# Kernel optimization log

Hardware: AMD Instinct MI355X
Metric: run time of the kernel (lower is better)

## Reference

```python
import jax, jax.numpy as jnp
import numpy as np
from jax import lax

NUM_CLASSES = 80
STRIDES = (8, 16, 32)
CENTER_RADIUS = 2.5
CANDIDATE_K = 10


def setup_inputs() -> dict:
    key = jax.random.key(0)
    ks = jax.random.split(key, 6)
    B, G, NGT = 32, 50, 20
    out0 = jax.random.normal(ks[0], (B, 85, 80, 80), jnp.float32)
    out1 = jax.random.normal(ks[1], (B, 85, 40, 40), jnp.float32)
    out2 = jax.random.normal(ks[2], (B, 85, 20, 20), jnp.float32)
    cls = jax.random.randint(ks[3], (B, G, 1), 0, NUM_CLASSES).astype(jnp.float32)
    cxcy = jax.random.uniform(ks[4], (B, G, 2), minval=32.0, maxval=608.0)
    wh = jax.random.uniform(ks[5], (B, G, 2), minval=16.0, maxval=128.0)
    labels = jnp.concatenate([cls, cxcy, wh], -1)
    valid = (jnp.arange(G) < NGT)[None, :, None]
    labels = labels * valid  # padded rows are all-zero, as the torch code expects
    return {"out0": out0, "out1": out1, "out2": out2, "labels": labels}


def _decode(out, stride):
    # out: [B, 85, H, W] -> [B, H*W, 85] with xy=(pred+grid)*stride, wh=exp(pred)*stride
    B, C, H, W = out.shape
    o = out.transpose(0, 2, 3, 1).reshape(B, H * W, C)
    yv, xv = jnp.meshgrid(jnp.arange(H), jnp.arange(W), indexing="ij")
    grid = jnp.stack([xv, yv], -1).reshape(H * W, 2).astype(out.dtype)
    xy = (o[..., :2] + grid) * stride
    wh = jnp.exp(o[..., 2:4]) * stride
    dec = jnp.concatenate([xy, wh, o[..., 4:]], -1)
    centers = (grid + 0.5) * stride
    strides = jnp.full((H * W,), float(stride), out.dtype)
    return dec, centers, strides


def _pairwise_iou(a, b):
    # a: [G,4] cxcywh, b: [A,4] cxcywh -> [G,A]
    tl = jnp.maximum(a[:, None, :2] - a[:, None, 2:] * 0.5, b[None, :, :2] - b[None, :, 2:] * 0.5)
    br = jnp.minimum(a[:, None, :2] + a[:, None, 2:] * 0.5, b[None, :, :2] + b[None, :, 2:] * 0.5)
    en = jnp.all(tl < br, -1).astype(a.dtype)
    inter = jnp.prod(br - tl, -1) * en
    area_a = a[:, 2] * a[:, 3]
    area_b = b[:, 2] * b[:, 3]
    return inter / (area_a[:, None] + area_b[None, :] - inter + 1e-12)


def _iou_loss(pred, tgt):
    # elementwise IoU loss (YOLOX IOUloss, loss_type='iou'): 1 - iou^2
    tl = jnp.maximum(pred[..., :2] - pred[..., 2:] * 0.5, tgt[..., :2] - tgt[..., 2:] * 0.5)
    br = jnp.minimum(pred[..., :2] + pred[..., 2:] * 0.5, tgt[..., :2] + tgt[..., 2:] * 0.5)
    en = jnp.all(tl < br, -1).astype(pred.dtype)
    inter = jnp.prod(jnp.clip(br - tl, 0.0), -1) * en
    union = pred[..., 2] * pred[..., 3] + tgt[..., 2] * tgt[..., 3] - inter + 1e-16
    iou = inter / union
    return 1.0 - iou * iou


def _bce_logits(x, y):
    return jnp.maximum(x, 0.0) - x * y + jnp.log1p(jnp.exp(-jnp.abs(x)))


def _assign(boxes, cls_logits, obj_logit, labels_b, centers, strides):
    # Per-image SimOTA. boxes [A,4], cls_logits [A,C], obj_logit [A], labels_b [G,5]
    G = labels_b.shape[0]
    gt_valid = labels_b.sum(-1) > 0                       # [G]
    gt_box = labels_b[:, 1:5]                             # [G,4] cxcywh
    gt_cls = labels_b[:, 0].astype(jnp.int32)
    cx, cy = centers[:, 0], centers[:, 1]
    # in-box test (strict, as min(delta)>0 in torch)
    in_box = ((cx[None] > gt_box[:, 0:1] - 0.5 * gt_box[:, 2:3])
              & (cx[None] < gt_box[:, 0:1] + 0.5 * gt_box[:, 2:3])
              & (cy[None] > gt_box[:, 1:2] - 0.5 * gt_box[:, 3:4])
              & (cy[None] < gt_box[:, 1:2] + 0.5 * gt_box[:, 3:4]))  # [G,A]
    rs = CENTER_RADIUS * strides[None]
    in_ctr = ((jnp.abs(cx[None] - gt_box[:, 0:1]) < rs)
              & (jnp.abs(cy[None] - gt_box[:, 1:2]) < rs))           # [G,A]
    fg = jnp.any((in_box | in_ctr) & gt_valid[:, None], axis=0)       # [A]
    geom = in_box & in_ctr                                            # is_in_boxes_and_center
    cand = fg[None, :] & gt_valid[:, None]                            # valid (gt, anchor) pairs

    iou = _pairwise_iou(gt_box, boxes)                                # [G,A]
    iou_m = jnp.where(cand, iou, 0.0)
    iou_cost = -jnp.log(iou + 1e-8)

    # cls cost without materializing [G,A,C]: p = sqrt(sig(cls)*sig(obj));
    # BCE(p, onehot(g)).sum(C) = -log p[g] + log(1-p[g]) - sum_c log(1-p[c])
    p = jnp.sqrt(jax.nn.sigmoid(cls_logits) * jax.nn.sigmoid(obj_logit)[:, None])  # [A,C]
    p = jnp.clip(p, 1e-7, 1.0 - 1e-6)
    logp = jnp.log(p)
    log1mp = jnp.log1p(-p)
    s = log1mp.sum(-1)                                                # [A]
    lp_g = jnp.take(logp, gt_cls, axis=1).T                           # [G,A]
    l1_g = jnp.take(log1mp, gt_cls, axis=1).T                         # [G,A]
    cls_cost = -lp_g + l1_g - s[None, :]

    cost = (cls_cost + 3.0 * iou_cost
            + 100000.0 * (~geom).astype(cost_dtype := boxes.dtype)
            + 1e9 * (~cand).astype(boxes.dtype))

    # dynamic-k: k_g = clamp(int(sum(topk10 ious)), 1)
    topk_ious = lax.top_k(iou_m, CANDIDATE_K)[0]                      # [G,10]
    dyn_k = jnp.clip(topk_ious.sum(-1).astype(jnp.int32), 1, None)    # [G]
    sorted_cost = jnp.sort(cost, axis=1)
    thr = jnp.take_along_axis(sorted_cost, (dyn_k - 1)[:, None], axis=1)
    match = (cost <= thr) & cand                                      # [G,A]

    # resolve anchors matched to multiple gts: keep global argmin-cost gt
    count = match.sum(0)                                              # [A]
    best_gt = jnp.argmin(cost, axis=0)                                # [A]
    keep = jnp.arange(G)[:, None] == best_gt[None, :]
    match = jnp.where(count[None, :] > 1, match & keep, match)

    fg_final = match.any(0)                                           # [A]
    matched_gt = jnp.argmax(match, axis=0)                            # [A]
    pred_iou = (match.astype(iou.dtype) * iou).sum(0)                 # [A]
    return fg_final, matched_gt, pred_iou, gt_valid


def _forward(out0, out1, out2, labels):
    decs, ctrs, strs = [], [], []
    for o, s in zip((out0, out1, out2), STRIDES):
        d, c, st = _decode(o, s)
        decs.append(d); ctrs.append(c); strs.append(st)
    outputs = jnp.concatenate(decs, axis=1)          # [B, A, 85]
    centers = jnp.concatenate(ctrs, axis=0)          # [A, 2]
    strides = jnp.concatenate(strs, axis=0)          # [A]

    bbox = outputs[..., :4]
    obj = outputs[..., 4]
    cls = outputs[..., 5:]

    assign = jax.vmap(_assign, in_axes=(0, 0, 0, 0, None, None))
    fg, mgt, piou, gt_valid = assign(
        lax.stop_gradient(bbox), lax.stop_gradient(cls),
        lax.stop_gradient(obj), lax.stop_gradient(labels), centers, strides)
    piou = lax.stop_gradient(piou)

    gt_box = lax.stop_gradient(labels[:, :, 1:5])
    reg_t = jnp.take_along_axis(gt_box, mgt[..., None], axis=1)       # [B,A,4]
    gt_cls = labels[..., 0].astype(jnp.int32)
    mcls = jnp.take_along_axis(gt_cls, mgt, axis=1)                   # [B,A]
    cls_t = jax.nn.one_hot(mcls, NUM_CLASSES, dtype=outputs.dtype) * piou[..., None]

    fgf = fg.astype(outputs.dtype)
    num_fg = jnp.maximum(fgf.sum(), 1.0)
    loss_iou = (_iou_loss(bbox, reg_t) * fgf).sum() / num_fg
    loss_obj = _bce_logits(obj, fgf).sum() / num_fg
    loss_cls = (_bce_logits(cls, cls_t).sum(-1) * fgf).sum() / num_fg
    return 5.0 * loss_iou + loss_obj + loss_cls


def reference(out0, out1, out2, labels):
    return _forward(out0, out1, out2, labels)
```

## Files before the change

kernel.cpp:

```cpp
#include <hip/hip_runtime.h>
#include <math.h>

#define B_  32
#define A_  8400
#define G_  50
#define NC_ 80
#define CLIPHI ((float)(1.0 - 1e-6))

#define ACC_NUMFG 0
#define ACC_IOU   32
#define ACC_OBJ0  64
#define ACC_OBJFG 96
#define ACC_CLS   128

struct AInfo { int lvl; int within; int w; int hw; float s; int x; int y; };

__device__ __forceinline__ AInfo anchor_info(int a) {
  AInfo r;
  if (a < 6400)      { r.lvl = 0; r.within = a;        r.w = 80; r.hw = 6400; r.s = 8.0f;  }
  else if (a < 8000) { r.lvl = 1; r.within = a - 6400; r.w = 40; r.hw = 1600; r.s = 16.0f; }
  else               { r.lvl = 2; r.within = a - 8000; r.w = 20; r.hw = 400;  r.s = 32.0f; }
  r.x = r.within % r.w; r.y = r.within / r.w;
  return r;
}

__device__ __forceinline__ const float* lvl_base(const float* o0, const float* o1,
                                                 const float* o2, int lvl) {
  return lvl == 0 ? o0 : (lvl == 1 ? o1 : o2);
}

__device__ __forceinline__ float2 cost_iou(
    float gx, float gy, float gw, float gh,
    float fx, float fy, float st,
    float4 bx, float ssum, float sobj, float clsv)
{
  float cx = (fx + 0.5f) * st;
  float cy = (fy + 0.5f) * st;
  bool in_box = (cx > gx - 0.5f*gw) && (cx < gx + 0.5f*gw) &&
                (cy > gy - 0.5f*gh) && (cy < gy + 0.5f*gh);
  float rs = 2.5f * st;
  bool in_ctr = (fabsf(cx - gx) < rs) && (fabsf(cy - gy) < rs);
  bool geom = in_box && in_ctr;
  float tlx = fmaxf(gx - gw*0.5f, bx.x - bx.z*0.5f);
  float tly = fmaxf(gy - gh*0.5f, bx.y - bx.w*0.5f);
  float brx = fminf(gx + gw*0.5f, bx.x + bx.z*0.5f);
  float bry = fminf(gy + gh*0.5f, bx.y + bx.w*0.5f);
  bool en = (tlx < brx) && (tly < bry);
  float inter = en ? (brx - tlx) * (bry - tly) : 0.0f;
  float iou = inter / (gw*gh + bx.z*bx.w - inter + 1e-12f);
  float iou_cost = -__logf(iou + 1e-8f);
  float sc = 1.0f / (1.0f + __expf(-clsv));
  float p = sqrtf(sc * sobj);
  p = fminf(fmaxf(p, 1e-7f), CLIPHI);
  float cls_cost = -__logf(p) + __logf(1.0f - p) - ssum;
  float cost = cls_cost + 3.0f * iou_cost;
  if (!geom) cost += 100000.0f;
  return make_float2(cost, iou);
}

__global__ __launch_bounds__(256)
void kA(const float* __restrict__ o0, const float* __restrict__ o1,
        const float* __restrict__ o2, const float* __restrict__ labels,
        float4* __restrict__ cBox, float4* __restrict__ cPack,
        int* __restrict__ ncandP, float* __restrict__ accP, int PAD)
{
  __shared__ float gl[G_], gr[G_], gtt[G_], gbb[G_], gcx[G_], gcy[G_];
  __shared__ int vflag[G_];
  __shared__ int nvgS;
  __shared__ float wsum[4];
  int b = blockIdx.y;
  int tid = threadIdx.x;
  if (tid < G_) {
    const float* L = labels + (size_t)b*G_*5 + tid*5;
    float l0=L[0], gx=L[1], gy=L[2], gw=L[3], gh=L[4];
    vflag[tid] = ((l0+gx+gy+gw+gh) > 0.0f) ? 1 : 0;
    gl[tid] = gx - 0.5f*gw; gr[tid] = gx + 0.5f*gw;
    gtt[tid] = gy - 0.5f*gh; gbb[tid] = gy + 0.5f*gh;
    gcx[tid] = gx; gcy[tid] = gy;
  }
  __syncthreads();
  if (tid == 0) {
    int n = 0;
    for (int g = 0; g < G_; g++) {
      if (vflag[g]) {
        gl[n]=gl[g]; gr[n]=gr[g]; gtt[n]=gtt[g]; gbb[n]=gbb[g];
        gcx[n]=gcx[g]; gcy[n]=gcy[g]; n++;
      }
    }
    nvgS = n;
  }
  __syncthreads();
  int nvg = nvgS;
  int a = blockIdx.x*256 + tid;
  bool inr = (a < A_);
  float objbce = 0.0f, v4 = 0.0f, so = 0.0f, ss = 0.0f;
  float4 bx = make_float4(0.f,0.f,0.f,0.f);
  bool anyfg = false;
  AInfo ai; const float* base = nullptr;
  if (inr) {
    ai = anchor_info(a);
    base = lvl_base(o0,o1,o2,ai.lvl) + (size_t)b*85*ai.hw + ai.within;
    float v0 = base[0];
    float v1 = base[(size_t)1*ai.hw];
    float v2 = base[(size_t)2*ai.hw];
    float v3 = base[(size_t)3*ai.hw];
    v4 = base[(size_t)4*ai.hw];
    bx.x = (v0 + (float)ai.x) * ai.s;
    bx.y = (v1 + (float)ai.y) * ai.s;
    bx.z = __expf(v2) * ai.s;
    bx.w = __expf(v3) * ai.s;
    objbce = fmaxf(v4, 0.0f) + __logf(1.0f + __expf(-fabsf(v4)));
    float cx = ((float)ai.x + 0.5f) * ai.s;
    float cy = ((float)ai.y + 0.5f) * ai.s;
    float rs = 2.5f * ai.s;
    for (int k = 0; k < nvg; k++) {
      bool in_box = (cx > gl[k]) && (cx < gr[k]) && (cy > gtt[k]) && (cy < gbb[k]);
      bool in_ctr = (fabsf(cx - gcx[k]) < rs) && (fabsf(cy - gcy[k]) < rs);
      if (in_box || in_ctr) { anyfg = true; break; }
    }
    so = 1.0f / (1.0f + __expf(-v4));
  }
  if (anyfg) {
    const float* q = base + (size_t)5*ai.hw;
    float s0=0,s1=0,s2=0,s3=0,s4=0,s5=0,s6=0,s7=0;
    for (int c = 0; c < NC_; c += 8) {
      float x0 = q[(size_t)(c+0)*ai.hw];
      float x1 = q[(size_t)(c+1)*ai.hw];
      float x2 = q[(size_t)(c+2)*ai.hw];
      float x3 = q[(size_t)(c+3)*ai.hw];
      float x4 = q[(size_t)(c+4)*ai.hw];
      float x5 = q[(size_t)(c+5)*ai.hw];
      float x6 = q[(size_t)(c+6)*ai.hw];
      float x7 = q[(size_t)(c+7)*ai.hw];
      #define TERM(xx, ss_) { \
        float sc = 1.0f/(1.0f+__expf(-(xx))); \
        float p = sqrtf(sc*so); \
        p = fminf(fmaxf(p,1e-7f), CLIPHI); \
        ss_ += __logf(1.0f - p); }
      TERM(x0,s0) TERM(x1,s1) TERM(x2,s2) TERM(x3,s3)
      TERM(x4,s4) TERM(x5,s5) TERM(x6,s6) TERM(x7,s7)
      #undef TERM
    }
    ss = ((s0+s1)+(s2+s3)) + ((s4+s5)+(s6+s7));
  }
  float v = objbce;
  for (int o = 32; o > 0; o >>= 1) v += __shfl_down(v, o, 64);
  if ((tid & 63) == 0) wsum[tid >> 6] = v;
  __syncthreads();
  if (tid == 0) atomicAdd(&accP[ACC_OBJ0], wsum[0]+wsum[1]+wsum[2]+wsum[3]);
  unsigned long long mm = __ballot(anyfg);
  int lane = tid & 63;
  int cnt = __popcll(mm);
  int b0 = 0;
  if (lane == 0 && cnt) b0 = atomicAdd(&ncandP[b*32], cnt);
  b0 = __shfl(b0, 0, 64);
  if (anyfg) {
    int pos = b0 + __popcll(mm & ((1ull << lane) - 1ull));
    if (pos < PAD) {
      cBox[b*A_ + pos]  = bx;
      cPack[b*A_ + pos] = make_float4(ss, so, __int_as_float(a), v4);
    }
  }
}

__global__ __launch_bounds__(256)
void kB(const float* __restrict__ o0, const float* __restrict__ o1,
        const float* __restrict__ o2, const float* __restrict__ labels,
        const float4* __restrict__ cBox, const float4* __restrict__ cPack,
        const int* __restrict__ ncandP, float* __restrict__ thrw,
        float* __restrict__ costM, int PAD)
{
  __shared__ float sh[256*10];
  __shared__ int s_dk;
  int g = blockIdx.x, b = blockIdx.y;
  int tid = threadIdx.x;
  const float* L = labels + (size_t)(b*G_ + g)*5;
  float l0=L[0], gx=L[1], gy=L[2], gw=L[3], gh=L[4];
  bool gvalid = (l0+gx+gy+gw+gh) > 0.0f;
  if (!gvalid) { if (tid==0) thrw[b*G_+g] = -3.0e38f; return; }
  int gcls = (int)l0;
  int nc = ncandP[b*32]; if (nc > PAD) nc = PAD;
  float* row = costM + ((size_t)b*G_ + g)*(size_t)PAD;
  float ti[10], tc[10];
  #pragma unroll
  for (int j=0;j<10;j++){ ti[j]=0.0f; tc[j]=3e38f; }
  for (int i = tid; i < nc; i += 256) {
    float4 bx = cBox[b*A_ + i];
    float4 pk = cPack[b*A_ + i];
    int a = __float_as_int(pk.z);
    AInfo ai = anchor_info(a);
    float clsv = lvl_base(o0,o1,o2,ai.lvl)[(size_t)(b*85 + 5 + gcls)*ai.hw + ai.within];
    float2 ci = cost_iou(gx,gy,gw,gh,(float)ai.x,(float)ai.y,ai.s,
                         bx, pk.x, pk.y, clsv);
    row[i] = ci.x;
    float v = ci.y;
    if (v > ti[9]) {
      #pragma unroll
      for (int j=0;j<10;j++){ float o=ti[j]; bool t=v>o; ti[j]=t?v:o; v=t?o:v; }
    }
    float c = ci.x;
    if (c < tc[9]) {
      #pragma unroll
      for (int j=0;j<10;j++){ float o=tc[j]; bool t=c<o; tc[j]=t?c:o; c=t?o:c; }
    }
  }
  #pragma unroll
  for (int j=0;j<10;j++) sh[tid*10+j] = ti[j];
  __syncthreads();
  for (int str=128; str>0; str>>=1) {
    if (tid < str) {
      float out[10]; int i=0, jj=0;
      float* Aa = &sh[tid*10]; float* Bb = &sh[(tid+str)*10];
      #pragma unroll
      for (int k=0;k<10;k++){ float va=Aa[i], vb=Bb[jj]; bool t=(va>=vb); out[k]=t?va:vb; if(t)i++; else jj++; }
      #pragma unroll
      for (int k=0;k<10;k++) Aa[k]=out[k];
    }
    __syncthreads();
  }
  if (tid==0) {
    float s10=0.0f;
    #pragma unroll
    for (int j=0;j<10;j++) s10 += sh[j];
    int dk = (int)s10; if (dk<1) dk=1; if (dk>10) dk=10;
    s_dk = dk;
  }
  __syncthreads();
  #pragma unroll
  for (int j=0;j<10;j++) sh[tid*10+j] = tc[j];
  __syncthreads();
  for (int str=128; str>0; str>>=1) {
    if (tid < str) {
      float out[10]; int i=0, jj=0;
      float* Aa = &sh[tid*10]; float* Bb = &sh[(tid+str)*10];
      #pragma unroll
      for (int k=0;k<10;k++){ float va=Aa[i], vb=Bb[jj]; bool t=(va<=vb); out[k]=t?va:vb; if(t)i++; else jj++; }
      #pragma unroll
      for (int k=0;k<10;k++) Aa[k]=out[k];
    }
    __syncthreads();
  }
  if (tid==0) thrw[b*G_+g] = sh[s_dk-1];
}

__global__ __launch_bounds__(256)
void kC(const float* __restrict__ o0, const float* __restrict__ o1,
        const float* __restrict__ o2, const float* __restrict__ labels,
        const float4* __restrict__ cBox, const float4* __restrict__ cPack,
        const int* __restrict__ ncandP, const float* __restrict__ thrw,
        const float* __restrict__ costM, float* __restrict__ accP, int PAD)
{
  int b = blockIdx.y;
  int nc = ncandP[b*32]; if (nc > PAD) nc = PAD;
  if (blockIdx.x*256 >= nc) return;
  __shared__ float labS[G_*5];
  __shared__ float thrS[G_];
  __shared__ int vgIdx[G_];
  __shared__ int nvgS;
  __shared__ float wpart[4][4];
  int tid = threadIdx.x;
  for (int i = tid; i < G_*5; i += 256) labS[i] = labels[(size_t)b*G_*5 + i];
  if (tid < G_) thrS[tid] = thrw[b*G_ + tid];
  __syncthreads();
  if (tid == 0) {
    int n = 0;
    for (int g = 0; g < G_; g++) {
      float s5 = labS[g*5]+labS[g*5+1]+labS[g*5+2]+labS[g*5+3]+labS[g*5+4];
      if (s5 > 0.0f) vgIdx[n++] = g;
    }
    nvgS = n;
  }
  __syncthreads();
  int nvg = nvgS;
  int i = blockIdx.x*256 + tid;
  float accPf=0.f, accIou=0.f, accObjx=0.f, accCls=0.f;
  if (i < nc) {
    const float* cm = costM + (size_t)b*G_*(size_t)PAD + i;
    float minc = 3e38f; int ming = 0;
    int cnt = 0; int firstg = -1;
    for (int k = 0; k < nvg; k++) {
      int g = vgIdx[k];
      float c = cm[(size_t)g*PAD];
      if (c < minc) { minc = c; ming = g; }
      if (c <= thrS[g]) { cnt++; if (firstg < 0) firstg = g; }
    }
    int mg = -1;
    if (cnt == 1)     mg = firstg;
    else if (cnt > 1) { if (minc <= thrS[ming]) mg = ming; }
    if (mg >= 0) {
      float4 bx = cBox[b*A_ + i];
      float4 pk = cPack[b*A_ + i];
      accPf = 1.0f;
      accObjx = pk.w;
      float tx=labS[mg*5+1], ty=labS[mg*5+2], tw=labS[mg*5+3], th=labS[mg*5+4];
      float tlx = fmaxf(tx - tw*0.5f, bx.x - bx.z*0.5f);
      float tly = fmaxf(ty - th*0.5f, bx.y - bx.w*0.5f);
      float brx = fminf(tx + tw*0.5f, bx.x + bx.z*0.5f);
      float bry = fminf(ty + th*0.5f, bx.y + bx.w*0.5f);
      bool en = (tlx < brx) && (tly < bry);
      float inter_p = en ? (brx - tlx) * (bry - tly) : 0.0f;
      float pi = inter_p / (tw*th + bx.z*bx.w - inter_p + 1e-12f);
      float iw = fmaxf(brx-tlx, 0.0f), ih = fmaxf(bry-tly, 0.0f);
      float inter = iw*ih * (en ? 1.0f : 0.0f);
      float uni = bx.z*bx.w + tw*th - inter + 1e-16f;
      float iou2 = inter/uni;
      accIou = 1.0f - iou2*iou2;
      int mcls = (int)labS[mg*5];
      int a = __float_as_int(pk.z);
      AInfo ai = anchor_info(a);
      const float* clsbase = lvl_base(o0,o1,o2,ai.lvl) + (size_t)(b*85 + 5)*ai.hw + ai.within;
      #pragma unroll 4
      for (int c = 0; c < NC_; c++) {
        float x = clsbase[(size_t)c * ai.hw];
        accCls += fmaxf(x,0.0f) - x*((c==mcls)?pi:0.0f) + __logf(1.0f + __expf(-fabsf(x)));
      }
    }
  }
  for (int o = 32; o > 0; o >>= 1) {
    accPf   += __shfl_down(accPf,   o, 64);
    accIou  += __shfl_down(accIou,  o, 64);
    accObjx += __shfl_down(accObjx, o, 64);
    accCls  += __shfl_down(accCls,  o, 64);
  }
  int lane = tid & 63, w = tid >> 6;
  if (lane == 0) { wpart[w][0]=accPf; wpart[w][1]=accIou; wpart[w][2]=accObjx; wpart[w][3]=accCls; }
  __syncthreads();
  if (tid == 0) {
    float s0=0.f,s1=0.f,s2=0.f,s3=0.f;
    for (int q=0;q<4;q++){ s0+=wpart[q][0]; s1+=wpart[q][1]; s2+=wpart[q][2]; s3+=wpart[q][3]; }
    if (s0!=0.f) atomicAdd(&accP[ACC_NUMFG], s0);
    if (s1!=0.f) atomicAdd(&accP[ACC_IOU],   s1);
    if (s2!=0.f) atomicAdd(&accP[ACC_OBJFG], s2);
    if (s3!=0.f) atomicAdd(&accP[ACC_CLS],   s3);
  }
}

__global__ void kE(const float* __restrict__ accP, float* __restrict__ out) {
  float nf = fmaxf(accP[ACC_NUMFG], 1.0f);
  out[0] = (5.0f*accP[ACC_IOU] + (accP[ACC_OBJ0] - accP[ACC_OBJFG]) + accP[ACC_CLS]) / nf;
}

extern "C" void kernel_launch(void* const* d_in, const int* in_sizes, int n_in,
                              void* d_out, int out_size, void* d_ws, size_t ws_size,
                              hipStream_t stream)
{
  const float* o0 = (const float*)d_in[0];
  const float* o1 = (const float*)d_in[1];
  const float* o2 = (const float*)d_in[2];
  const float* labels = (const float*)d_in[3];
  char* w = (char*)d_ws;
  size_t off = 0;
  auto alloc = [&](size_t bytes) -> void* {
    void* p = w + off; off += (bytes + 255) & ~(size_t)255; return p;
  };
  float4* cBox  = (float4*)alloc(sizeof(float4)*(size_t)B_*A_);
  float4* cPack = (float4*)alloc(sizeof(float4)*(size_t)B_*A_);
  float*  thrw  = (float*) alloc(sizeof(float)*(size_t)B_*G_);
  int*    ncandP= (int*)   alloc(sizeof(int)*B_*32);
  float*  accP  = (float*) alloc(sizeof(float)*256);
  size_t avail = (ws_size > off) ? (ws_size - off) : 0;
  size_t padMax = avail / ((size_t)B_*G_*sizeof(float));
  int PAD = (int)(padMax > 8448 ? 8448 : (padMax & ~(size_t)255));
  if (PAD < 256) PAD = 256;
  float* costM = (float*)alloc(sizeof(float)*(size_t)B_*G_*(size_t)PAD);

  hipMemsetAsync(ncandP, 0, sizeof(int)*B_*32, stream);
  hipMemsetAsync(accP, 0, sizeof(float)*256, stream);

  dim3 grdA((A_+255)/256, B_);
  kA<<<grdA, 256, 0, stream>>>(o0,o1,o2,labels,cBox,cPack,ncandP,accP,PAD);
  kB<<<dim3(G_,B_), 256, 0, stream>>>(o0,o1,o2,labels,cBox,cPack,ncandP,thrw,costM,PAD);
  kC<<<grdA, 256, 0, stream>>>(o0,o1,o2,labels,cBox,cPack,ncandP,thrw,costM,accP,PAD);
  kE<<<1,1,0,stream>>>(accP, (float*)d_out);
}
```

Baseline: 202.8 us.

## Move class log-sum and per-GT class gathers into a compacted-candidate kernel

A new kernel kS runs only over the compacted foreground candidates. It computes the 80-class log(1-p) sum there instead of in the divergent branch of kA. It also gathers each valid GT's class logit into a dense per-GT buffer, so kB reads contiguous values instead of doing scattered strided loads into the raw outputs. kC's grid is sized by the candidate pad instead of all anchors. The extra buffer halves the cap on stored candidates, which risks truncation if an image has more candidates than the new limit.

```diff
diff --git a/kernel.cpp b/kernel.cpp
--- a/kernel.cpp
+++ b/kernel.cpp
@@ -92,14 +92,12 @@
   __syncthreads();
   int nvg = nvgS;
   int a = blockIdx.x*256 + tid;
-  bool inr = (a < A_);
-  float objbce = 0.0f, v4 = 0.0f, so = 0.0f, ss = 0.0f;
+  float objbce = 0.0f, v4 = 0.0f, so = 0.0f;
   float4 bx = make_float4(0.f,0.f,0.f,0.f);
   bool anyfg = false;
-  AInfo ai; const float* base = nullptr;
-  if (inr) {
-    ai = anchor_info(a);
-    base = lvl_base(o0,o1,o2,ai.lvl) + (size_t)b*85*ai.hw + ai.within;
+  if (a < A_) {
+    AInfo ai = anchor_info(a);
+    const float* base = lvl_base(o0,o1,o2,ai.lvl) + (size_t)b*85*ai.hw + ai.within;
     float v0 = base[0];
     float v1 = base[(size_t)1*ai.hw];
     float v2 = base[(size_t)2*ai.hw];
@@ -120,29 +118,6 @@
     }
     so = 1.0f / (1.0f + __expf(-v4));
   }
-  if (anyfg) {
-    const float* q = base + (size_t)5*ai.hw;
-    float s0=0,s1=0,s2=0,s3=0,s4=0,s5=0,s6=0,s7=0;
-    for (int c = 0; c < NC_; c += 8) {
-      float x0 = q[(size_t)(c+0)*ai.hw];
-      float x1 = q[(size_t)(c+1)*ai.hw];
-      float x2 = q[(size_t)(c+2)*ai.hw];
-      float x3 = q[(size_t)(c+3)*ai.hw];
-      float x4 = q[(size_t)(c+4)*ai.hw];
-      float x5 = q[(size_t)(c+5)*ai.hw];
-      float x6 = q[(size_t)(c+6)*ai.hw];
-      float x7 = q[(size_t)(c+7)*ai.hw];
-      #define TERM(xx, ss_) { \
-        float sc = 1.0f/(1.0f+__expf(-(xx))); \
-        float p = sqrtf(sc*so); \
-        p = fminf(fmaxf(p,1e-7f), CLIPHI); \
-        ss_ += __logf(1.0f - p); }
-      TERM(x0,s0) TERM(x1,s1) TERM(x2,s2) TERM(x3,s3)
-      TERM(x4,s4) TERM(x5,s5) TERM(x6,s6) TERM(x7,s7)
-      #undef TERM
-    }
-    ss = ((s0+s1)+(s2+s3)) + ((s4+s5)+(s6+s7));
-  }
   float v = objbce;
   for (int o = 32; o > 0; o >>= 1) v += __shfl_down(v, o, 64);
   if ((tid & 63) == 0) wsum[tid >> 6] = v;
@@ -158,17 +133,73 @@
     int pos = b0 + __popcll(mm & ((1ull << lane) - 1ull));
     if (pos < PAD) {
       cBox[b*A_ + pos]  = bx;
-      cPack[b*A_ + pos] = make_float4(ss, so, __int_as_float(a), v4);
+      cPack[b*A_ + pos] = make_float4(0.0f, so, __int_as_float(a), v4);
     }
   }
 }
 
 __global__ __launch_bounds__(256)
-void kB(const float* __restrict__ o0, const float* __restrict__ o1,
+void kS(const float* __restrict__ o0, const float* __restrict__ o1,
         const float* __restrict__ o2, const float* __restrict__ labels,
+        float4* __restrict__ cPack, const int* __restrict__ ncandP,
+        float* __restrict__ clsGT, int PAD)
+{
+  __shared__ int vgIdx[G_], vgCls[G_];
+  __shared__ int nvgS;
+  int b = blockIdx.y;
+  int nc = ncandP[b*32]; if (nc > PAD) nc = PAD;
+  if (blockIdx.x*256 >= nc) return;
+  int tid = threadIdx.x;
+  if (tid == 0) {
+    int n = 0;
+    for (int g = 0; g < G_; g++) {
+      const float* L = labels + (size_t)b*G_*5 + g*5;
+      float s5 = L[0]+L[1]+L[2]+L[3]+L[4];
+      if (s5 > 0.0f) { vgIdx[n] = g; vgCls[n] = (int)L[0]; n++; }
+    }
+    nvgS = n;
+  }
+  __syncthreads();
+  int nvg = nvgS;
+  int i = blockIdx.x*256 + tid;
+  if (i >= nc) return;
+  float4 pk = cPack[b*A_ + i];
+  float so = pk.y;
+  int a = __float_as_int(pk.z);
+  AInfo ai = anchor_info(a);
+  const float* q = lvl_base(o0,o1,o2,ai.lvl) + (size_t)(b*85 + 5)*ai.hw + ai.within;
+  float s0=0,s1=0,s2=0,s3=0,s4=0,s5=0,s6=0,s7=0;
+  for (int c = 0; c < NC_; c += 8) {
+    float x0 = q[(size_t)(c+0)*ai.hw];
+    float x1 = q[(size_t)(c+1)*ai.hw];
+    float x2 = q[(size_t)(c+2)*ai.hw];
+    float x3 = q[(size_t)(c+3)*ai.hw];
+    float x4 = q[(size_t)(c+4)*ai.hw];
+    float x5 = q[(size_t)(c+5)*ai.hw];
+    float x6 = q[(size_t)(c+6)*ai.hw];
+    float x7 = q[(size_t)(c+7)*ai.hw];
+    #define TERM(xx, ss_) { \
+      float sc = 1.0f/(1.0f+__expf(-(xx))); \
+      float p = sqrtf(sc*so); \
+      p = fminf(fmaxf(p,1e-7f), CLIPHI); \
+      ss_ += __logf(1.0f - p); }
+    TERM(x0,s0) TERM(x1,s1) TERM(x2,s2) TERM(x3,s3)
+    TERM(x4,s4) TERM(x5,s5) TERM(x6,s6) TERM(x7,s7)
+    #undef TERM
+  }
+  float ss = ((s0+s1)+(s2+s3)) + ((s4+s5)+(s6+s7));
+  ((float*)&cPack[b*A_ + i])[0] = ss;
+  for (int k = 0; k < nvg; k++) {
+    float clsv = q[(size_t)vgCls[k] * ai.hw];
+    clsGT[((size_t)b*G_ + vgIdx[k])*(size_t)PAD + i] = clsv;
+  }
+}
+
+__global__ __launch_bounds__(256)
+void kB(const float* __restrict__ labels,
         const float4* __restrict__ cBox, const float4* __restrict__ cPack,
         const int* __restrict__ ncandP, float* __restrict__ thrw,
-        float* __restrict__ costM, int PAD)
+        float* __restrict__ costM, const float* __restrict__ clsGT, int PAD)
 {
   __shared__ float sh[256*10];
   __shared__ int s_dk;
@@ -178,18 +209,18 @@
   float l0=L[0], gx=L[1], gy=L[2], gw=L[3], gh=L[4];
   bool gvalid = (l0+gx+gy+gw+gh) > 0.0f;
   if (!gvalid) { if (tid==0) thrw[b*G_+g] = -3.0e38f; return; }
-  int gcls = (int)l0;
   int nc = ncandP[b*32]; if (nc > PAD) nc = PAD;
   float* row = costM + ((size_t)b*G_ + g)*(size_t)PAD;
+  const float* crow = clsGT + ((size_t)b*G_ + g)*(size_t)PAD;
   float ti[10], tc[10];
   #pragma unroll
   for (int j=0;j<10;j++){ ti[j]=0.0f; tc[j]=3e38f; }
   for (int i = tid; i < nc; i += 256) {
     float4 bx = cBox[b*A_ + i];
     float4 pk = cPack[b*A_ + i];
+    float clsv = crow[i];
     int a = __float_as_int(pk.z);
     AInfo ai = anchor_info(a);
-    float clsv = lvl_base(o0,o1,o2,ai.lvl)[(size_t)(b*85 + 5 + gcls)*ai.hw + ai.within];
     float2 ci = cost_iou(gx,gy,gw,gh,(float)ai.x,(float)ai.y,ai.s,
                          bx, pk.x, pk.y, clsv);
     row[i] = ci.x;
@@ -359,17 +390,20 @@
   int*    ncandP= (int*)   alloc(sizeof(int)*B_*32);
   float*  accP  = (float*) alloc(sizeof(float)*256);
   size_t avail = (ws_size > off) ? (ws_size - off) : 0;
-  size_t padMax = avail / ((size_t)B_*G_*sizeof(float));
-  int PAD = (int)(padMax > 8448 ? 8448 : (padMax & ~(size_t)255));
+  size_t padMax = avail / (2 * (size_t)B_*G_*sizeof(float));
+  int PAD = (int)(padMax > 4352 ? 4352 : (padMax & ~(size_t)255));
   if (PAD < 256) PAD = 256;
   float* costM = (float*)alloc(sizeof(float)*(size_t)B_*G_*(size_t)PAD);
+  float* clsGT = (float*)alloc(sizeof(float)*(size_t)B_*G_*(size_t)PAD);
 
   hipMemsetAsync(ncandP, 0, sizeof(int)*B_*32, stream);
   hipMemsetAsync(accP, 0, sizeof(float)*256, stream);
 
   dim3 grdA((A_+255)/256, B_);
+  dim3 grdP((PAD+255)/256, B_);
   kA<<<grdA, 256, 0, stream>>>(o0,o1,o2,labels,cBox,cPack,ncandP,accP,PAD);
-  kB<<<dim3(G_,B_), 256, 0, stream>>>(o0,o1,o2,labels,cBox,cPack,ncandP,thrw,costM,PAD);
-  kC<<<grdA, 256, 0, stream>>>(o0,o1,o2,labels,cBox,cPack,ncandP,thrw,costM,accP,PAD);
+  kS<<<grdP, 256, 0, stream>>>(o0,o1,o2,labels,cPack,ncandP,clsGT,PAD);
+  kB<<<dim3(G_,B_), 256, 0, stream>>>(labels,cBox,cPack,ncandP,thrw,costM,clsGT,PAD);
+  kC<<<grdP, 256, 0, stream>>>(o0,o1,o2,labels,cBox,cPack,ncandP,thrw,costM,accP,PAD);
   kE<<<1,1,0,stream>>>(accP, (float*)d_out);
 }
```

After: 215.8 us. 6.4% more time.
